# Performance work log

Hardware: AMD Instinct MI355X
Metric: run time of the kernel (lower is better)

## Reference

```python
import jax, jax.numpy as jnp
import numpy as np

H = 1024

def setup_inputs() -> dict:
    key = jax.random.key(0)
    ks = jax.random.split(key, 7)
    B, S = 64, 2048
    decoder_hidden = jax.random.normal(ks[0], (B, H), dtype=jnp.float32)
    encoder_outputs = jax.random.normal(ks[1], (B, S, H), dtype=jnp.float32)
    sc = 1.0 / np.sqrt(H)
    W1_w = jax.random.normal(ks[2], (H, H), dtype=jnp.float32) * sc
    W1_b = jax.random.normal(ks[3], (H,), dtype=jnp.float32) * sc
    W2_w = jax.random.normal(ks[4], (H, H), dtype=jnp.float32) * sc
    W2_b = jax.random.normal(ks[5], (H,), dtype=jnp.float32) * sc
    v_w = jax.random.normal(ks[6], (H,), dtype=jnp.float32) * sc
    return {"decoder_hidden": decoder_hidden, "encoder_outputs": encoder_outputs,
            "W1_w": W1_w, "W1_b": W1_b, "W2_w": W2_w, "W2_b": W2_b, "v_w": v_w}

def reference(decoder_hidden, encoder_outputs, W1_w, W1_b, W2_w, W2_b, v_w):
    # enc proj: [B,S,H] @ [H,H] ; dec proj: [B,H] @ [H,H], broadcast over S
    enc_proj = jnp.einsum('bsh,hk->bsk', encoder_outputs, W1_w) + W1_b
    dec_proj = decoder_hidden @ W2_w + W2_b  # [B,H]
    e = jnp.tanh(enc_proj + dec_proj[:, None, :])  # [B,S,H]
    scores = jnp.einsum('bsh,h->bs', e, v_w)  # [B,S]
    attn_weights = jax.nn.softmax(scores, axis=1)
    context = jnp.einsum('bs,bsh->bh', attn_weights, encoder_outputs)
    return (context, attn_weights)
```

## Files before the change

kernel.cpp:

```cpp
#include <hip/hip_runtime.h>
#include <hip/hip_bf16.h>
#include <hip/hip_fp16.h>

#define HDIM 1024
#define BATCH 64
#define SEQ 2048
#define MTOT (BATCH*SEQ)
#define BM 128
#define BN 256
#define BK 64
#define NKT (HDIM/BK)
#define NNT (HDIM/BN)

typedef float f32x4 __attribute__((ext_vector_type(4)));
typedef _Float16 half8 __attribute__((ext_vector_type(8)));

static __device__ __forceinline__ void gload_lds16(const void* g, void* l) {
  __builtin_amdgcn_global_load_lds((const __attribute__((address_space(1))) void*)g,
                                   (__attribute__((address_space(3))) void*)l, 16, 0, 0);
}

__global__ void k_w1t(const float* __restrict__ W1, unsigned short* __restrict__ W1T) {
  __shared__ float tile[64][65];
  int h0 = blockIdx.x * 64, k0 = blockIdx.y * 64;
  int t = threadIdx.x;
#pragma unroll
  for (int j = 0; j < 4; ++j) {
    int q = j * 256 + t, r = q >> 4, c = (q & 15) * 4;
    float4 v = *(const float4*)(W1 + (size_t)(h0 + r) * HDIM + k0 + c);
    tile[r][c + 0] = v.x; tile[r][c + 1] = v.y; tile[r][c + 2] = v.z; tile[r][c + 3] = v.w;
  }
  __syncthreads();
#pragma unroll
  for (int j = 0; j < 4; ++j) {
    int q = j * 256 + t, r = q >> 4, c = (q & 15) * 4;
    union { _Float16 h[4]; ushort4 u; } cv;
    cv.h[0] = (_Float16)tile[c + 0][r];
    cv.h[1] = (_Float16)tile[c + 1][r];
    cv.h[2] = (_Float16)tile[c + 2][r];
    cv.h[3] = (_Float16)tile[c + 3][r];
    *(ushort4*)(W1T + (size_t)(k0 + r) * HDIM + h0 + c) = cv.u;
  }
}

__global__ void k_decproj(const float* __restrict__ dh, const float* __restrict__ W2,
                          const float* __restrict__ W2b, float* __restrict__ dp) {
  __shared__ float drow[HDIM];
  int b = blockIdx.x, t = threadIdx.x;
#pragma unroll
  for (int j = 0; j < 4; ++j) drow[j * 256 + t] = dh[(size_t)b * HDIM + j * 256 + t];
  __syncthreads();
  f32x4 acc = {0.f, 0.f, 0.f, 0.f};
#pragma unroll 16
  for (int h = 0; h < HDIM; ++h) {
    float d = drow[h];
    f32x4 w = *(const f32x4*)(W2 + (size_t)h * HDIM + t * 4);
    acc += w * d;
  }
  acc += *(const f32x4*)(W2b + t * 4);
  *(f32x4*)(dp + (size_t)b * HDIM + t * 4) = acc;
}

__global__ __launch_bounds__(512, 4) void k_scores(
    const float* __restrict__ E, const unsigned short* __restrict__ W1T,
    const float* __restrict__ W1b, const float* __restrict__ dp,
    const float* __restrict__ vw, float* __restrict__ spart) {
  __shared__ __align__(16) _Float16 As[BM * BK];
  __shared__ __align__(16) unsigned short Bs[BN * BK];
  float (*scr)[4] = (float(*)[4])As;

  int t = threadIdx.x;
  int bid = blockIdx.x;
  int xcd = bid & 7;
  int q = bid >> 3;
  int mt = (xcd << 7) + (q >> 2);
  int nt = q & 3;
  int m0 = mt * BM, n0 = nt * BN;
  int b = m0 >> 11;

  int lane = t & 63, wid = t >> 6;
  int wr = wid >> 2, wc = wid & 3;
  int l15 = lane & 15, l4 = lane >> 4;

  f32x4 acc[4][4];
#pragma unroll
  for (int i = 0; i < 4; ++i)
#pragma unroll
    for (int j = 0; j < 4; ++j) acc[i][j] = {0.f, 0.f, 0.f, 0.f};

  int ar = t >> 4;
  int ac = (t & 15) * 4;
  int aswz = (((ac >> 3) ^ (ar & 7)) << 4) + ((ac & 7) << 1);
  const float* Ab = E + (size_t)m0 * HDIM;

  float4 areg[4];
#pragma unroll
  for (int j = 0; j < 4; ++j)
    areg[j] = *(const float4*)(Ab + (size_t)(j * 32 + ar) * HDIM + ac);

  for (int kt = 0; kt < NKT; ++kt) {
#pragma unroll
    for (int j = 0; j < 4; ++j) {
      int chunk = wid * 4 + j;
      int row = chunk * 8 + (lane >> 3);
      int u = (lane & 7) ^ (lane >> 3);
      const unsigned short* g = W1T + (size_t)(n0 + row) * HDIM + kt * BK + u * 8;
      gload_lds16(g, (char*)Bs + (size_t)chunk * 1024);
    }

#pragma unroll
    for (int j = 0; j < 4; ++j) {
      union { _Float16 h[4]; unsigned long long u64; } cv;
      cv.h[0] = (_Float16)areg[j].x; cv.h[1] = (_Float16)areg[j].y;
      cv.h[2] = (_Float16)areg[j].z; cv.h[3] = (_Float16)areg[j].w;
      *(unsigned long long*)((char*)As + (j * 32 + ar) * 128 + aswz) = cv.u64;
    }

    __syncthreads();

    int ktn = ((kt + 1) & (NKT - 1)) * BK;
#pragma unroll
    for (int j = 0; j < 4; ++j)
      areg[j] = *(const float4*)(Ab + (size_t)(j * 32 + ar) * HDIM + ktn + ac);

    __builtin_amdgcn_s_setprio(1);
#pragma unroll
    for (int ks = 0; ks < 2; ++ks) {
      half8 af[4], bf[4];
#pragma unroll
      for (int mi = 0; mi < 4; ++mi) {
        int row = wr * 64 + mi * 16 + l15;
        af[mi] = *(const half8*)((const char*)As + row * 128 + (((ks * 4 + l4) ^ (row & 7)) << 4));
      }
#pragma unroll
      for (int ni = 0; ni < 4; ++ni) {
        int row = wc * 64 + ni * 16 + l15;
        bf[ni] = *(const half8*)((const char*)Bs + row * 128 + (((ks * 4 + l4) ^ (row & 7)) << 4));
      }
#pragma unroll
      for (int mi = 0; mi < 4; ++mi)
#pragma unroll
        for (int ni = 0; ni < 4; ++ni)
          acc[mi][ni] = __builtin_amdgcn_mfma_f32_16x16x32_f16(af[mi], bf[ni], acc[mi][ni], 0, 0, 0);
    }
    __builtin_amdgcn_s_setprio(0);

    __syncthreads();
  }

  float bias_l[4], v_l[4];
#pragma unroll
  for (int ni = 0; ni < 4; ++ni) {
    int k = n0 + wc * 64 + ni * 16 + l15;
    bias_l[ni] = W1b[k] + dp[(size_t)b * HDIM + k];
    v_l[ni] = vw[k];
  }
#pragma unroll
  for (int mi = 0; mi < 4; ++mi) {
#pragma unroll
    for (int r = 0; r < 4; ++r) {
      float s = 0.f;
#pragma unroll
      for (int ni = 0; ni < 4; ++ni) {
        float x = acc[mi][ni][r] + bias_l[ni];
        float ex = __expf(2.f * x);
        float th = 1.f - 2.f / (ex + 1.f);
        s += th * v_l[ni];
      }
      s += __shfl_xor(s, 1); s += __shfl_xor(s, 2);
      s += __shfl_xor(s, 4); s += __shfl_xor(s, 8);
      if (l15 == 0) scr[wr * 64 + mi * 16 + l4 * 4 + r][wc] = s;
    }
  }
  __syncthreads();
  if (t < BM) {
    f32x4 p = *(const f32x4*)scr[t];
    spart[((size_t)m0 + t) * NNT + nt] = (p[0] + p[1]) + (p[2] + p[3]);
  }
}

__global__ void k_softmax(const float* __restrict__ spart, float* __restrict__ attn) {
  __shared__ float sc[SEQ];
  __shared__ float red[8];
  int b = blockIdx.x, t = threadIdx.x;
  float mx = -1e30f;
#pragma unroll
  for (int j = 0; j < 8; ++j) {
    int s = j * 256 + t;
    f32x4 x = *(const f32x4*)(spart + ((size_t)b * SEQ + s) * NNT);
    float v = (x[0] + x[1]) + (x[2] + x[3]);
    sc[s] = v;
    mx = fmaxf(mx, v);
  }
  for (int m = 1; m < 64; m <<= 1) mx = fmaxf(mx, __shfl_xor(mx, m));
  if ((t & 63) == 0) red[t >> 6] = mx;
  __syncthreads();
  mx = fmaxf(fmaxf(red[0], red[1]), fmaxf(red[2], red[3]));
  float w[8]; float sum = 0.f;
#pragma unroll
  for (int j = 0; j < 8; ++j) {
    float e = __expf(sc[j * 256 + t] - mx);
    w[j] = e; sum += e;
  }
  for (int m = 1; m < 64; m <<= 1) sum += __shfl_xor(sum, m);
  if ((t & 63) == 0) red[4 + (t >> 6)] = sum;
  __syncthreads();
  float inv = 1.f / (red[4] + red[5] + red[6] + red[7]);
#pragma unroll
  for (int j = 0; j < 8; ++j)
    attn[(size_t)b * SEQ + j * 256 + t] = w[j] * inv;
}

__global__ void k_ctx_part(const float* __restrict__ E, const float* __restrict__ attn,
                           float* __restrict__ cpart, int rpc) {
  int b = blockIdx.y, ch = blockIdx.x, nch = gridDim.x;
  int t = threadIdx.x;
  const float* wrow = attn + (size_t)b * SEQ + (size_t)ch * rpc;
  const float* Eb = E + ((size_t)b * SEQ + (size_t)ch * rpc) * HDIM;
  f32x4 acc = {0.f, 0.f, 0.f, 0.f};
#pragma unroll 4
  for (int s = 0; s < rpc; ++s) {
    float w = wrow[s];
    f32x4 e = *(const f32x4*)(Eb + (size_t)s * HDIM + t * 4);
    acc += e * w;
  }
  *(f32x4*)(cpart + ((size_t)b * nch + ch) * HDIM + t * 4) = acc;
}

__global__ void k_ctx_reduce(const float* __restrict__ cpart, float* __restrict__ ctx, int nch) {
  int idx = blockIdx.x * 256 + threadIdx.x;
  int b = idx >> 10, k = idx & 1023;
  float s = 0.f;
  for (int c = 0; c < nch; ++c) s += cpart[((size_t)(b * nch + c)) * HDIM + k];
  ctx[idx] = s;
}

extern "C" void kernel_launch(void* const* d_in, const int* in_sizes, int n_in,
                              void* d_out, int out_size, void* d_ws, size_t ws_size,
                              hipStream_t stream) {
  const float* dh  = (const float*)d_in[0];
  const float* E   = (const float*)d_in[1];
  const float* W1w = (const float*)d_in[2];
  const float* W1b = (const float*)d_in[3];
  const float* W2w = (const float*)d_in[4];
  const float* W2b = (const float*)d_in[5];
  const float* vw  = (const float*)d_in[6];
  float* out  = (float*)d_out;
  float* ctx  = out;
  float* attn = out + BATCH * HDIM;

  char* ws = (char*)d_ws;
  unsigned short* W1T = (unsigned short*)ws;
  float* dp    = (float*)(ws + (2u << 20));
  float* spart = (float*)(ws + (2u << 20) + (256u << 10));
  float* cpart = (float*)(ws + (6u << 20) + (256u << 10));

  size_t need32 = (6u << 20) + (256u << 10) + (size_t)BATCH * 32 * HDIM * 4;
  int nch = (ws_size >= need32) ? 32 : 16;
  int rpc = SEQ / nch;

  k_w1t<<<dim3(16, 16), 256, 0, stream>>>(W1w, W1T);
  k_decproj<<<BATCH, 256, 0, stream>>>(dh, W2w, W2b, dp);
  k_scores<<<(MTOT / BM) * NNT, 512, 0, stream>>>(E, W1T, W1b, dp, vw, spart);
  k_softmax<<<BATCH, 256, 0, stream>>>(spart, attn);
  k_ctx_part<<<dim3(nch, BATCH), 256, 0, stream>>>(E, attn, cpart, rpc);
  k_ctx_reduce<<<256, 256, 0, stream>>>(cpart, ctx, nch);
}
```

Baseline: 521.5 us.

## Write fp16 copy of encoder outputs in scores kernel for context pass

The scores GEMM already converts the fp32 encoder outputs to fp16 for its A tiles. The tiles with nt==0 now also write that fp16 data to a workspace copy. The context kernel then reads the fp16 copy instead of the fp32 tensor, halving its read traffic. In exchange the scores kernel gains an extra 256MB of global writes, and the path only runs when the workspace is large enough. The context result also loses precision from reading fp16 values.

```diff
diff --git a/kernel.cpp b/kernel.cpp
--- a/kernel.cpp
+++ b/kernel.cpp
@@ -14,6 +14,7 @@
 
 typedef float f32x4 __attribute__((ext_vector_type(4)));
 typedef _Float16 half8 __attribute__((ext_vector_type(8)));
+typedef _Float16 half4v __attribute__((ext_vector_type(4)));
 
 static __device__ __forceinline__ void gload_lds16(const void* g, void* l) {
   __builtin_amdgcn_global_load_lds((const __attribute__((address_space(1))) void*)g,
@@ -64,7 +65,8 @@
 __global__ __launch_bounds__(512, 4) void k_scores(
     const float* __restrict__ E, const unsigned short* __restrict__ W1T,
     const float* __restrict__ W1b, const float* __restrict__ dp,
-    const float* __restrict__ vw, float* __restrict__ spart) {
+    const float* __restrict__ vw, float* __restrict__ spart,
+    unsigned short* __restrict__ E16, int we16) {
   __shared__ __align__(16) _Float16 As[BM * BK];
   __shared__ __align__(16) unsigned short Bs[BN * BK];
   float (*scr)[4] = (float(*)[4])As;
@@ -92,6 +94,7 @@
   int ac = (t & 15) * 4;
   int aswz = (((ac >> 3) ^ (ar & 7)) << 4) + ((ac & 7) << 1);
   const float* Ab = E + (size_t)m0 * HDIM;
+  int wr16 = we16 && (nt == 0);
 
   float4 areg[4];
 #pragma unroll
@@ -114,6 +117,8 @@
       cv.h[0] = (_Float16)areg[j].x; cv.h[1] = (_Float16)areg[j].y;
       cv.h[2] = (_Float16)areg[j].z; cv.h[3] = (_Float16)areg[j].w;
       *(unsigned long long*)((char*)As + (j * 32 + ar) * 128 + aswz) = cv.u64;
+      if (wr16)
+        *(unsigned long long*)(E16 + (size_t)(m0 + j * 32 + ar) * HDIM + kt * BK + ac) = cv.u64;
     }
 
     __syncthreads();
@@ -223,6 +228,25 @@
     float w = wrow[s];
     f32x4 e = *(const f32x4*)(Eb + (size_t)s * HDIM + t * 4);
     acc += e * w;
+  }
+  *(f32x4*)(cpart + ((size_t)b * nch + ch) * HDIM + t * 4) = acc;
+}
+
+__global__ void k_ctx_part16(const unsigned short* __restrict__ E16, const float* __restrict__ attn,
+                             float* __restrict__ cpart, int rpc) {
+  int b = blockIdx.y, ch = blockIdx.x, nch = gridDim.x;
+  int t = threadIdx.x;
+  const float* wrow = attn + (size_t)b * SEQ + (size_t)ch * rpc;
+  const unsigned short* Eb = E16 + ((size_t)b * SEQ + (size_t)ch * rpc) * HDIM;
+  f32x4 acc = {0.f, 0.f, 0.f, 0.f};
+#pragma unroll 4
+  for (int s = 0; s < rpc; ++s) {
+    float w = wrow[s];
+    half4v e = *(const half4v*)(Eb + (size_t)s * HDIM + t * 4);
+    acc[0] += w * (float)e[0];
+    acc[1] += w * (float)e[1];
+    acc[2] += w * (float)e[2];
+    acc[3] += w * (float)e[3];
   }
   *(f32x4*)(cpart + ((size_t)b * nch + ch) * HDIM + t * 4) = acc;
 }
@@ -254,15 +278,22 @@
   float* dp    = (float*)(ws + (2u << 20));
   float* spart = (float*)(ws + (2u << 20) + (256u << 10));
   float* cpart = (float*)(ws + (6u << 20) + (256u << 10));
-
-  size_t need32 = (6u << 20) + (256u << 10) + (size_t)BATCH * 32 * HDIM * 4;
+  unsigned short* E16 = (unsigned short*)(ws + (14u << 20) + (256u << 10));
+
+  size_t need32  = (6u << 20) + (256u << 10) + (size_t)BATCH * 32 * HDIM * 4;
+  size_t needE16 = (14u << 20) + (256u << 10) + (size_t)MTOT * HDIM * 2;
   int nch = (ws_size >= need32) ? 32 : 16;
   int rpc = SEQ / nch;
+  int use16 = (ws_size >= needE16) ? 1 : 0;
 
   k_w1t<<<dim3(16, 16), 256, 0, stream>>>(W1w, W1T);
   k_decproj<<<BATCH, 256, 0, stream>>>(dh, W2w, W2b, dp);
-  k_scores<<<(MTOT / BM) * NNT, 512, 0, stream>>>(E, W1T, W1b, dp, vw, spart);
+  k_scores<<<(MTOT / BM) * NNT, 512, 0, stream>>>(E, W1T, W1b, dp, vw, spart,
+                                                  use16 ? E16 : W1T, use16);
   k_softmax<<<BATCH, 256, 0, stream>>>(spart, attn);
-  k_ctx_part<<<dim3(nch, BATCH), 256, 0, stream>>>(E, attn, cpart, rpc);
+  if (use16)
+    k_ctx_part16<<<dim3(nch, BATCH), 256, 0, stream>>>(E16, attn, cpart, rpc);
+  else
+    k_ctx_part<<<dim3(nch, BATCH), 256, 0, stream>>>(E, attn, cpart, rpc);
   k_ctx_reduce<<<256, 256, 0, stream>>>(cpart, ctx, nch);
 }
```

New measurement: 525.9 us. No clear change (+0.8%).
